# Kernel tuning notes

Measured on AMD Instinct MI355X. Metric: run time of the kernel, lower is better.

## Reference

```python
import jax, jax.numpy as jnp
import numpy as np

B, N1, N2 = 4, 16384, 4096   # scenes, fine points/scene, coarse points/scene
CIN, COUT = 512, 256
K = 3
EPS_BN = 1e-5
EPS_D = 1e-8


def setup_inputs() -> dict:
    key = jax.random.key(0)
    ks = jax.random.split(key, 6)
    return {
        "point_1": jax.random.uniform(ks[0], (B * N1, 3), dtype=jnp.float32),
        "feat_1": jax.random.normal(ks[1], (B * N1, COUT), dtype=jnp.float32) * 0.1,
        "point_2": jax.random.uniform(ks[2], (B * N2, 3), dtype=jnp.float32),
        "feat_2": jax.random.normal(ks[3], (B * N2, CIN), dtype=jnp.float32) * 0.1,
        "W1": jax.random.normal(ks[4], (COUT, COUT), dtype=jnp.float32) / np.sqrt(COUT).astype(np.float32),
        "b1": jnp.zeros((COUT,), jnp.float32),
        "g1": jnp.ones((COUT,), jnp.float32),
        "beta1": jnp.zeros((COUT,), jnp.float32),
        "W2": jax.random.normal(ks[5], (CIN, COUT), dtype=jnp.float32) / np.sqrt(CIN).astype(np.float32),
        "b2": jnp.zeros((COUT,), jnp.float32),
        "g2": jnp.ones((COUT,), jnp.float32),
        "beta2": jnp.zeros((COUT,), jnp.float32),
        # equal-sized segments: row_splits = [0, N, 2N, ...]
        "row_splits_1": jnp.arange(B + 1, dtype=jnp.int32) * N1,
        "row_splits_2": jnp.arange(B + 1, dtype=jnp.int32) * N2,
    }


def _bn(x, gamma, beta):
    # BatchNorm1d, training mode (biased variance, as in torch)
    mu = x.mean(0)
    var = x.var(0)
    return gamma * (x - mu) * jax.lax.rsqrt(var + EPS_BN) + beta


def reference(point_1, feat_1, point_2, feat_2,
              W1, b1, g1, beta1, W2, b2, g2, beta2,
              row_splits_1, row_splits_2):
    # linear1(feat_1): Linear + BN + ReLU
    f1 = jax.nn.relu(_bn(feat_1 @ W1 + b1, g1, beta1))          # [B*N1, COUT]
    # linear2(feat_2): Linear + BN + ReLU
    f2 = jax.nn.relu(_bn(feat_2 @ W2 + b2, g2, beta2))          # [B*N2, COUT]

    # batched KNN (equal row_splits -> reshape into [B, n, 3])
    q = point_1.reshape(B, N1, 3)
    p = point_2.reshape(B, N2, 3)
    d2 = ((q * q).sum(-1)[:, :, None]
          + (p * p).sum(-1)[:, None, :]
          - 2.0 * jnp.einsum("bnd,bmd->bnm", q, p))             # [B, N1, N2] squared dists
    neg_d, idx = jax.lax.top_k(-d2, K)                           # [B, N1, K]
    dist = jnp.maximum(-neg_d, 0.0)

    # inverse-distance weights (knn search is non-differentiable in the original)
    recip = 1.0 / (dist + EPS_D)
    w = jax.lax.stop_gradient(recip / recip.sum(-1, keepdims=True))  # [B, N1, K]

    # gather + weighted sum (three-interpolate)
    f2b = f2.reshape(B, N2, COUT)
    gathered = f2b[jnp.arange(B)[:, None, None], idx]            # [B, N1, K, COUT]
    interp = (gathered * w[..., None]).sum(2).reshape(B * N1, COUT)

    return f1 + interp
```

## Files before the change

kernel.cpp:

```cpp
#include <hip/hip_runtime.h>
#include <hip/hip_bf16.h>
#include <math.h>

#define N1R 65536
#define N2R 16384
#define NPB 4096
#define NQB 16384
#define CC  256
#define KC  64
#define NCELL 512
#define GRID_FAIL_R2 0.015625f

typedef __attribute__((ext_vector_type(4))) float v4f;
typedef __attribute__((ext_vector_type(8))) short v8s;

typedef const __attribute__((address_space(1))) float glb_f32;
typedef __attribute__((address_space(3))) float lds_f32;

static __device__ __forceinline__ void gload16(const float* g, float* l) {
    __builtin_amdgcn_global_load_lds((glb_f32*)g, (lds_f32*)l, 16, 0, 0);
}

static __device__ __forceinline__ short f2bs(float f) {
    union { __hip_bfloat16 h; short s; } u;
    u.h = __float2bfloat16(f);
    return u.s;
}

static __device__ __forceinline__ int cell_of(float x, float y, float z) {
    const int cx = min(7, (int)(x * 8.0f));
    const int cy = min(7, (int)(y * 8.0f));
    const int cz = min(7, (int)(z * 8.0f));
    return (cz << 6) | (cy << 3) | cx;
}

static __device__ __forceinline__ void ins3(float d, int si,
    float& b0, float& b1, float& b2, int& i0, int& i1, int& i2)
{
    const bool lt0 = (d < b0) | ((d == b0) & (si < i0));
    const bool lt1 = (d < b1) | ((d == b1) & (si < i1));
    const bool lt2 = (d < b2) | ((d == b2) & (si < i2));
    b2 = lt1 ? b1 : (lt2 ? d : b2);   i2 = lt1 ? i1 : (lt2 ? si : i2);
    b1 = lt0 ? b0 : (lt1 ? d : b1);   i1 = lt0 ? i0 : (lt1 ? si : i1);
    b0 = lt0 ? d  : b0;               i0 = lt0 ? si : i0;
}

__global__ __launch_bounds__(256)
void wtrans_kernel(const float* __restrict__ W, short* __restrict__ WT, int Kd)
{
    const int i = blockIdx.x * 256 + threadIdx.x;
    const int k = i >> 8;
    const int n = i & 255;
    WT[(size_t)n * Kd + k] = f2bs(W[i]);
}

__global__ __launch_bounds__(256)
void paug_count_kernel(const float* __restrict__ p2, float4* __restrict__ paug,
                       int* __restrict__ counts_p)
{
#pragma clang fp contract(off)
    const int i = blockIdx.x * 256 + threadIdx.x;
    const float x = p2[(size_t)i * 3 + 0];
    const float y = p2[(size_t)i * 3 + 1];
    const float z = p2[(size_t)i * 3 + 2];
    float4 v;
    v.x = x; v.y = y; v.z = z;
    v.w = (x * x + y * y) + z * z;
    paug[i] = v;
    const int b = i >> 12;
    atomicAdd(&counts_p[b * NCELL + cell_of(x, y, z)], 1);
}

__global__ __launch_bounds__(256)
void qcount_kernel(const float* __restrict__ p1, int* __restrict__ counts_q)
{
    const int i = blockIdx.x * 256 + threadIdx.x;
    const float x = p1[(size_t)i * 3 + 0];
    const float y = p1[(size_t)i * 3 + 1];
    const float z = p1[(size_t)i * 3 + 2];
    const int b = i >> 14;
    atomicAdd(&counts_q[b * NCELL + cell_of(x, y, z)], 1);
}

__global__ __launch_bounds__(512)
void prefix_kernel(const int* __restrict__ counts_p, int* __restrict__ cursors_p,
                   int* __restrict__ starts_p,
                   const int* __restrict__ counts_q, int* __restrict__ cursors_q)
{
    __shared__ int sc[512];
    const int t = threadIdx.x;
    for (int a = 0; a < 8; ++a) {
        const int b = a & 3;
        const int* cnt = (a < 4) ? counts_p + b * NCELL : counts_q + b * NCELL;
        const int v = cnt[t];
        sc[t] = v;
        __syncthreads();
        for (int off = 1; off < 512; off <<= 1) {
            const int add = (t >= off) ? sc[t - off] : 0;
            __syncthreads();
            sc[t] += add;
            __syncthreads();
        }
        const int incl = sc[t];
        const int excl = incl - v;
        if (a < 4) {
            starts_p[b * 513 + t] = excl;
            if (t == 511) starts_p[b * 513 + 512] = incl;
            cursors_p[b * NCELL + t] = excl;
        } else {
            cursors_q[b * NCELL + t] = excl;
        }
        __syncthreads();
    }
}

__global__ __launch_bounds__(256)
void scatter_p_kernel(const float4* __restrict__ paug, int* __restrict__ cursors,
                      float4* __restrict__ sortedP, unsigned short* __restrict__ sIdx)
{
    const int i = blockIdx.x * 256 + threadIdx.x;
    const float4 v = paug[i];
    const int b = i >> 12;
    const int cell = cell_of(v.x, v.y, v.z);
    const int pos = atomicAdd(&cursors[b * NCELL + cell], 1);
    sortedP[(size_t)b * NPB + pos] = v;
    sIdx[(size_t)b * NPB + pos] = (unsigned short)(i & 4095);
}

__global__ __launch_bounds__(256)
void scatter_q_kernel(const float* __restrict__ p1, int* __restrict__ cursors,
                      unsigned short* __restrict__ qlist)
{
    const int i = blockIdx.x * 256 + threadIdx.x;
    const float x = p1[(size_t)i * 3 + 0];
    const float y = p1[(size_t)i * 3 + 1];
    const float z = p1[(size_t)i * 3 + 2];
    const int b = i >> 14;
    const int cell = cell_of(x, y, z);
    const int pos = atomicAdd(&cursors[b * NCELL + cell], 1);
    qlist[(size_t)b * NQB + pos] = (unsigned short)(i & 16383);
}

__global__ __launch_bounds__(256)
void gemm_fused_kernel(const float* __restrict__ X,
                       const short* __restrict__ WT,
                       const float* __restrict__ bias,
                       float* __restrict__ Y,
                       float* __restrict__ sum, float* __restrict__ sumsq,
                       int Kdim)
{
    __shared__ float As[2][128 * KC];

    const int bm0 = blockIdx.x * 128;
    const int bn0 = blockIdx.y * 128;
    const int tid  = threadIdx.x;
    const int wave = tid >> 6;
    const int lane = tid & 63;
    const int wm0 = (wave >> 1) * 64;
    const int wn0 = (wave & 1) * 64;
    const int col = lane & 15, quad = lane >> 4;

    const int srow4 = lane >> 4;
    const int sslot = lane & 15;

    v4f acc[4][4];
#pragma unroll
    for (int i = 0; i < 4; ++i)
#pragma unroll
        for (int j = 0; j < 4; ++j) acc[i][j] = (v4f){0.f, 0.f, 0.f, 0.f};

    const short* wbase = WT + (size_t)(bn0 + wn0 + col) * Kdim + quad * 8;

#pragma unroll
    for (int j = 0; j < 8; ++j) {
        const int r = (wave * 8 + j) * 4 + srow4;
        const float* g = X + (size_t)(bm0 + r) * Kdim + ((sslot ^ (r & 7)) << 2);
        gload16(g, &As[0][(wave * 8 + j) * 256]);
    }

    const int NC = Kdim / KC;
    for (int c = 0; c < NC; ++c) {
        const int k0 = c * KC;
        __syncthreads();
        const float* bufc = As[c & 1];

        v8s bf[4][2];
#pragma unroll
        for (int ni = 0; ni < 4; ++ni)
#pragma unroll
            for (int ks = 0; ks < 2; ++ks)
                bf[ni][ks] = *(const v8s*)(wbase + (size_t)(ni * 16) * Kdim + k0 + ks * 32);

        if (c + 1 < NC) {
            float* bufn = As[(c + 1) & 1];
#pragma unroll
            for (int j = 0; j < 8; ++j) {
                const int r = (wave * 8 + j) * 4 + srow4;
                const float* g = X + (size_t)(bm0 + r) * Kdim + (k0 + KC) + ((sslot ^ (r & 7)) << 2);
                gload16(g, &bufn[(wave * 8 + j) * 256]);
            }
        }

#pragma unroll
        for (int ks = 0; ks < 2; ++ks) {
            const int sbase = ks * 8 + quad * 2;
            v8s a[4];
#pragma unroll
            for (int mi = 0; mi < 4; ++mi) {
                const int m = wm0 + mi * 16 + col;
                const float* rowp = bufc + m * KC;
                const v4f pa = *(const v4f*)(rowp + ((sbase ^ (m & 7)) << 2));
                const v4f pb = *(const v4f*)(rowp + (((sbase + 1) ^ (m & 7)) << 2));
                v8s t;
#pragma unroll
                for (int j = 0; j < 4; ++j) { t[j] = f2bs(pa[j]); t[j + 4] = f2bs(pb[j]); }
                a[mi] = t;
            }
#pragma unroll
            for (int mi = 0; mi < 4; ++mi)
#pragma unroll
                for (int ni = 0; ni < 4; ++ni)
                    acc[mi][ni] = __builtin_amdgcn_mfma_f32_16x16x32_bf16(a[mi], bf[ni][ks], acc[mi][ni], 0, 0, 0);
        }
    }

#pragma unroll
    for (int ni = 0; ni < 4; ++ni) {
        const int n = bn0 + wn0 + ni * 16 + col;
        const float bv = bias[n];
        float s = 0.f, q = 0.f;
#pragma unroll
        for (int mi = 0; mi < 4; ++mi) {
            const int m = bm0 + wm0 + mi * 16 + quad * 4;
#pragma unroll
            for (int r = 0; r < 4; ++r) {
                const float y = acc[mi][ni][r] + bv;
                Y[(size_t)(m + r) * CC + n] = y;
                s += y; q += y * y;
            }
        }
        s += __shfl_xor(s, 16); q += __shfl_xor(q, 16);
        s += __shfl_xor(s, 32); q += __shfl_xor(q, 32);
        if (quad == 0) { atomicAdd(&sum[n], s); atomicAdd(&sumsq[n], q); }
    }
}

__global__ __launch_bounds__(512)
void finalize_kernel(const float* __restrict__ sums,
                     const float* __restrict__ g1, const float* __restrict__ be1,
                     const float* __restrict__ g2, const float* __restrict__ be2,
                     float* __restrict__ ac)
{
    const int t = threadIdx.x;
    const int c = t & 255;
    const int which = t >> 8;
    const float* s = sums + which * 512;
    const double n = which ? (double)N2R : (double)N1R;
    const double mu = (double)s[c] / n;
    const double var = (double)s[c + 256] / n - mu * mu;
    const float g  = which ? g2[c]  : g1[c];
    const float be = which ? be2[c] : be1[c];
    const double a  = (double)g / sqrt(var + 1e-5);
    const double cv = (double)be - a * mu;
    ac[which * 512 + c]       = (float)a;
    ac[which * 512 + 256 + c] = (float)cv;
}

__global__ __launch_bounds__(256)
void knn_grid_kernel(const float* __restrict__ p1,
                     const float4* __restrict__ sortedP,
                     const unsigned short* __restrict__ sIdx16,
                     const int* __restrict__ starts_p,
                     const unsigned short* __restrict__ qlist,
                     int* __restrict__ idx_out, float* __restrict__ w_out,
                     int* __restrict__ failCount, int* __restrict__ failList)
{
#pragma clang fp contract(off)
    __shared__ float4 sP[NPB];
    __shared__ unsigned short sI[NPB];
    __shared__ int sS[513];
    __shared__ float mD[128 * 3];
    __shared__ int   mI[128 * 3];

    const int b = blockIdx.x >> 7;
    const int slot0 = (blockIdx.x & 127) * 128;
    const int tid = threadIdx.x;
    const int lq = tid & 127;
    const int half = tid >> 7;

    {
        const float4* gp = sortedP + (size_t)b * NPB;
        for (int i = tid; i < NPB; i += 256) sP[i] = gp[i];
        const unsigned int* gi = (const unsigned int*)(sIdx16 + (size_t)b * NPB);
        unsigned int* li = (unsigned int*)sI;
        for (int i = tid; i < NPB / 2; i += 256) li[i] = gi[i];
        const int* gs = starts_p + b * 513;
        for (int i = tid; i < 513; i += 256) sS[i] = gs[i];
    }

    const int q = qlist[(size_t)b * NQB + slot0 + lq];
    const int qid = b * NQB + q;
    const float qx = p1[(size_t)qid * 3 + 0];
    const float qy = p1[(size_t)qid * 3 + 1];
    const float qz = p1[(size_t)qid * 3 + 2];
    const float qq = (qx * qx + qy * qy) + qz * qz;
    const int cqx = min(7, (int)(qx * 8.0f));
    const int cqy = min(7, (int)(qy * 8.0f));
    const int cqz = min(7, (int)(qz * 8.0f));

    __syncthreads();

    float b0 = 3.0e38f, b1 = 3.0e38f, b2 = 3.0e38f;
    int i0 = 0x7fffffff, i1 = 0x7fffffff, i2 = 0x7fffffff;

    int n = 0;
    for (int dz = -1; dz <= 1; ++dz)
        for (int dy = -1; dy <= 1; ++dy)
            for (int dx = -1; dx <= 1; ++dx, ++n) {
                if (half ? (n < 14) : (n >= 14)) continue;
                const int cz = cqz + dz, cy = cqy + dy, cx = cqx + dx;
                if (((unsigned)cz | (unsigned)cy | (unsigned)cx) > 7u) continue;
                const int cell = (cz << 6) | (cy << 3) | cx;
                const int ks = sS[cell], ke = sS[cell + 1];
                for (int k = ks; k < ke; ++k) {
                    const float4 P = sP[k];
                    const int si = sI[k];
                    const float dot = fmaf(qz, P.z, fmaf(qy, P.y, qx * P.x));
                    const float d = fmaf(-2.0f, dot, qq + P.w);
                    ins3(d, si, b0, b1, b2, i0, i1, i2);
                }
            }

    if (half) {
        mD[lq * 3 + 0] = b0; mD[lq * 3 + 1] = b1; mD[lq * 3 + 2] = b2;
        mI[lq * 3 + 0] = i0; mI[lq * 3 + 1] = i1; mI[lq * 3 + 2] = i2;
    }
    __syncthreads();
    if (!half) {
#pragma unroll
        for (int r = 0; r < 3; ++r)
            ins3(mD[lq * 3 + r], mI[lq * 3 + r], b0, b1, b2, i0, i1, i2);

        if (!(b2 < GRID_FAIL_R2)) {
            const int p = atomicAdd(failCount, 1);
            if (p < N1R) failList[p] = qid;
        }
        const float r0 = 1.0f / (fmaxf(b0, 0.0f) + 1e-8f);
        const float r1 = 1.0f / (fmaxf(b1, 0.0f) + 1e-8f);
        const float r2 = 1.0f / (fmaxf(b2, 0.0f) + 1e-8f);
        const float rs = (r0 + r1) + r2;
        idx_out[(size_t)qid * 3 + 0] = i0;
        idx_out[(size_t)qid * 3 + 1] = i1;
        idx_out[(size_t)qid * 3 + 2] = i2;
        w_out[(size_t)qid * 3 + 0] = r0 / rs;
        w_out[(size_t)qid * 3 + 1] = r1 / rs;
        w_out[(size_t)qid * 3 + 2] = r2 / rs;
    }
}

__global__ __launch_bounds__(256)
void knn_bf_kernel(const float* __restrict__ p1,
                   const float4* __restrict__ paug,
                   const int* __restrict__ failCount,
                   const int* __restrict__ failList,
                   int* __restrict__ idx_out, float* __restrict__ w_out)
{
#pragma clang fp contract(off)
    const int nf = min(*failCount, N1R);
    const int gw = (blockIdx.x * 256 + threadIdx.x) >> 6;
    const int lane = threadIdx.x & 63;
    const int nw = (gridDim.x * 256) >> 6;

    for (int fi = gw; fi < nf; fi += nw) {
        const int qid = failList[fi];
        const int b = qid >> 14;
        const float qx = p1[(size_t)qid * 3 + 0];
        const float qy = p1[(size_t)qid * 3 + 1];
        const float qz = p1[(size_t)qid * 3 + 2];
        const float qq = (qx * qx + qy * qy) + qz * qz;

        float b0 = 3.0e38f, b1 = 3.0e38f, b2 = 3.0e38f;
        int i0 = 0x7fffffff, i1 = 0x7fffffff, i2 = 0x7fffffff;

        const float4* pb = paug + (size_t)b * NPB;
        for (int j = lane; j < NPB; j += 64) {
            const float4 P = pb[j];
            const float dot = fmaf(qz, P.z, fmaf(qy, P.y, qx * P.x));
            const float d = fmaf(-2.0f, dot, qq + P.w);
            ins3(d, j, b0, b1, b2, i0, i1, i2);
        }
        for (int m = 1; m < 64; m <<= 1) {
            const float c0 = __shfl_xor(b0, m), c1 = __shfl_xor(b1, m), c2 = __shfl_xor(b2, m);
            const int j0 = __shfl_xor(i0, m), j1 = __shfl_xor(i1, m), j2 = __shfl_xor(i2, m);
            ins3(c0, j0, b0, b1, b2, i0, i1, i2);
            ins3(c1, j1, b0, b1, b2, i0, i1, i2);
            ins3(c2, j2, b0, b1, b2, i0, i1, i2);
        }
        if (lane == 0) {
            const float r0 = 1.0f / (fmaxf(b0, 0.0f) + 1e-8f);
            const float r1 = 1.0f / (fmaxf(b1, 0.0f) + 1e-8f);
            const float r2 = 1.0f / (fmaxf(b2, 0.0f) + 1e-8f);
            const float rs = (r0 + r1) + r2;
            idx_out[(size_t)qid * 3 + 0] = i0;
            idx_out[(size_t)qid * 3 + 1] = i1;
            idx_out[(size_t)qid * 3 + 2] = i2;
            w_out[(size_t)qid * 3 + 0] = r0 / rs;
            w_out[(size_t)qid * 3 + 1] = r1 / rs;
            w_out[(size_t)qid * 3 + 2] = r2 / rs;
        }
    }
}

__global__ __launch_bounds__(256)
void final_kernel(float* __restrict__ Y1out,
                  const float* __restrict__ Y2raw,
                  const float* __restrict__ ac,
                  const int* __restrict__ idx, const float* __restrict__ w)
{
    const int r = blockIdx.x * 4 + (threadIdx.x >> 6);
    const int cg = threadIdx.x & 63;
    const int b = r >> 14;

    v4f a1 = *(const v4f*)(ac + cg * 4);
    v4f c1 = *(const v4f*)(ac + 256 + cg * 4);
    v4f a2 = *(const v4f*)(ac + 512 + cg * 4);
    v4f c2 = *(const v4f*)(ac + 768 + cg * 4);
    v4f y = *(const v4f*)(Y1out + (size_t)r * CC + cg * 4);
    v4f s;
#pragma unroll
    for (int j = 0; j < 4; ++j)
        s[j] = fmaxf(fmaf(a1[j], y[j], c1[j]), 0.f);

    const int*   ir = idx + (size_t)r * 3;
    const float* wr = w   + (size_t)r * 3;
#pragma unroll
    for (int k = 0; k < 3; ++k) {
        const int id = ir[k];
        const float wk = wr[k];
        v4f g = *(const v4f*)(Y2raw + ((size_t)(b * NPB + id)) * CC + cg * 4);
#pragma unroll
        for (int j = 0; j < 4; ++j) {
            const float gv = fmaxf(fmaf(a2[j], g[j], c2[j]), 0.f);
            s[j] = fmaf(wk, gv, s[j]);
        }
    }
    *(v4f*)(Y1out + (size_t)r * CC + cg * 4) = s;
}

extern "C" void kernel_launch(void* const* d_in, const int* in_sizes, int n_in,
                              void* d_out, int out_size, void* d_ws, size_t ws_size,
                              hipStream_t stream)
{
    const float* point1 = (const float*)d_in[0];
    const float* feat1  = (const float*)d_in[1];
    const float* point2 = (const float*)d_in[2];
    const float* feat2  = (const float*)d_in[3];
    const float* W1     = (const float*)d_in[4];
    const float* b1     = (const float*)d_in[5];
    const float* g1     = (const float*)d_in[6];
    const float* beta1  = (const float*)d_in[7];
    const float* W2     = (const float*)d_in[8];
    const float* b2     = (const float*)d_in[9];
    const float* g2     = (const float*)d_in[10];
    const float* beta2  = (const float*)d_in[11];

    float* Y1 = (float*)d_out;

    char* ws = (char*)d_ws;
    float*          Y2       = (float*)ws;
    float*          stats    = (float*)(ws + (size_t)16777216);
    int*            counts_p = (int*)  (ws + (size_t)16781312);
    int*            counts_q = (int*)  (ws + (size_t)16789504);
    int*            failCnt  = (int*)  (ws + (size_t)16797696);
    int*            cursors_p= (int*)  (ws + (size_t)16801792);
    int*            cursors_q= (int*)  (ws + (size_t)16809984);
    int*            starts_p = (int*)  (ws + (size_t)16818176);
    float*          ac       = (float*)(ws + (size_t)16826624);
    unsigned short* sIdx16   = (unsigned short*)(ws + (size_t)16830720);
    unsigned short* qlist    = (unsigned short*)(ws + (size_t)16863488);
    int*            failList = (int*)  (ws + (size_t)16994560);
    float4*         sortedP  = (float4*)(ws + (size_t)17256704);
    int*            idxb     = (int*)  (ws + (size_t)17518848);
    float*          wb       = (float*)(ws + (size_t)18305280);
    short*          WT1      = (short*)(ws + (size_t)19091712);
    short*          WT2      = (short*)(ws + (size_t)19222784);
    float4*         paug     = (float4*)(ws + (size_t)19484928);

    hipMemsetAsync(stats, 0, 24576, stream);

    wtrans_kernel<<<256, 256, 0, stream>>>(W1, WT1, 256);
    wtrans_kernel<<<512, 256, 0, stream>>>(W2, WT2, 512);

    paug_count_kernel<<<N2R / 256, 256, 0, stream>>>(point2, paug, counts_p);
    qcount_kernel<<<N1R / 256, 256, 0, stream>>>(point1, counts_q);
    prefix_kernel<<<1, 512, 0, stream>>>(counts_p, cursors_p, starts_p, counts_q, cursors_q);
    scatter_p_kernel<<<N2R / 256, 256, 0, stream>>>(paug, cursors_p, sortedP, sIdx16);
    scatter_q_kernel<<<N1R / 256, 256, 0, stream>>>(point1, cursors_q, qlist);

    gemm_fused_kernel<<<dim3(N1R / 128, 2), 256, 0, stream>>>(feat1, WT1, b1, Y1,
                                                              stats + 0,   stats + 256, 256);
    gemm_fused_kernel<<<dim3(N2R / 128, 2), 256, 0, stream>>>(feat2, WT2, b2, Y2,
                                                              stats + 512, stats + 768, 512);

    finalize_kernel<<<1, 512, 0, stream>>>(stats, g1, beta1, g2, beta2, ac);

    knn_grid_kernel<<<512, 256, 0, stream>>>(point1, sortedP, sIdx16, starts_p,
                                             qlist, idxb, wb, failCnt, failList);
    knn_bf_kernel<<<256, 256, 0, stream>>>(point1, paug, failCnt, failList, idxb, wb);

    final_kernel<<<N1R / 4, 256, 0, stream>>>(Y1, Y2, ac, idxb, wb);
}
```

Measured before the change: 350.3 us.

## Load GEMM A operand directly from global into registers, drop LDS staging

The fused GEMM+BN-stats kernel no longer stages the fp32 activation tile in double-buffered LDS via global_load_lds. Each lane now reads its own A fragment straight from global memory, converts it to bf16 and feeds the MFMA. K is also made a template parameter so the loop unrolls at compile time. This removes LDS traffic, barriers and the LDS footprint, which may help occupancy. In exchange, the two column-halves of the grid (blockIdx.y) and the two waves sharing a row range within a block each fetch the same X rows, so global/L2 traffic rises, and latency hiding now depends on unrolling.

Result: slower. 365.3 us (+4.3%).

```diff
diff --git a/kernel.cpp b/kernel.cpp
--- a/kernel.cpp
+++ b/kernel.cpp
@@ -7,19 +7,11 @@
 #define NPB 4096
 #define NQB 16384
 #define CC  256
-#define KC  64
 #define NCELL 512
 #define GRID_FAIL_R2 0.015625f
 
 typedef __attribute__((ext_vector_type(4))) float v4f;
 typedef __attribute__((ext_vector_type(8))) short v8s;
-
-typedef const __attribute__((address_space(1))) float glb_f32;
-typedef __attribute__((address_space(3))) float lds_f32;
-
-static __device__ __forceinline__ void gload16(const float* g, float* l) {
-    __builtin_amdgcn_global_load_lds((glb_f32*)g, (lds_f32*)l, 16, 0, 0);
-}
 
 static __device__ __forceinline__ short f2bs(float f) {
     union { __hip_bfloat16 h; short s; } u;
@@ -141,87 +133,55 @@
     qlist[(size_t)b * NQB + pos] = (unsigned short)(i & 16383);
 }
 
+template<int KD>
 __global__ __launch_bounds__(256)
 void gemm_fused_kernel(const float* __restrict__ X,
                        const short* __restrict__ WT,
                        const float* __restrict__ bias,
                        float* __restrict__ Y,
-                       float* __restrict__ sum, float* __restrict__ sumsq,
-                       int Kdim)
-{
-    __shared__ float As[2][128 * KC];
-
+                       float* __restrict__ sum, float* __restrict__ sumsq)
+{
     const int bm0 = blockIdx.x * 128;
     const int bn0 = blockIdx.y * 128;
-    const int tid  = threadIdx.x;
-    const int wave = tid >> 6;
-    const int lane = tid & 63;
+    const int wave = threadIdx.x >> 6;
+    const int lane = threadIdx.x & 63;
     const int wm0 = (wave >> 1) * 64;
     const int wn0 = (wave & 1) * 64;
     const int col = lane & 15, quad = lane >> 4;
 
-    const int srow4 = lane >> 4;
-    const int sslot = lane & 15;
-
     v4f acc[4][4];
 #pragma unroll
     for (int i = 0; i < 4; ++i)
 #pragma unroll
         for (int j = 0; j < 4; ++j) acc[i][j] = (v4f){0.f, 0.f, 0.f, 0.f};
 
-    const short* wbase = WT + (size_t)(bn0 + wn0 + col) * Kdim + quad * 8;
-
-#pragma unroll
-    for (int j = 0; j < 8; ++j) {
-        const int r = (wave * 8 + j) * 4 + srow4;
-        const float* g = X + (size_t)(bm0 + r) * Kdim + ((sslot ^ (r & 7)) << 2);
-        gload16(g, &As[0][(wave * 8 + j) * 256]);
-    }
-
-    const int NC = Kdim / KC;
-    for (int c = 0; c < NC; ++c) {
-        const int k0 = c * KC;
-        __syncthreads();
-        const float* bufc = As[c & 1];
-
-        v8s bf[4][2];
+    const short* wbase = WT + (size_t)(bn0 + wn0 + col) * KD + quad * 8;
+    const float* xbase = X + (size_t)(bm0 + wm0 + col) * KD + quad * 8;
+
+#pragma unroll 2
+    for (int k0 = 0; k0 < KD; k0 += 32) {
+        v8s bf[4];
 #pragma unroll
         for (int ni = 0; ni < 4; ++ni)
-#pragma unroll
-            for (int ks = 0; ks < 2; ++ks)
-                bf[ni][ks] = *(const v8s*)(wbase + (size_t)(ni * 16) * Kdim + k0 + ks * 32);
-
-        if (c + 1 < NC) {
-            float* bufn = As[(c + 1) & 1];
-#pragma unroll
-            for (int j = 0; j < 8; ++j) {
-                const int r = (wave * 8 + j) * 4 + srow4;
-                const float* g = X + (size_t)(bm0 + r) * Kdim + (k0 + KC) + ((sslot ^ (r & 7)) << 2);
-                gload16(g, &bufn[(wave * 8 + j) * 256]);
-            }
-        }
-
-#pragma unroll
-        for (int ks = 0; ks < 2; ++ks) {
-            const int sbase = ks * 8 + quad * 2;
-            v8s a[4];
-#pragma unroll
-            for (int mi = 0; mi < 4; ++mi) {
-                const int m = wm0 + mi * 16 + col;
-                const float* rowp = bufc + m * KC;
-                const v4f pa = *(const v4f*)(rowp + ((sbase ^ (m & 7)) << 2));
-                const v4f pb = *(const v4f*)(rowp + (((sbase + 1) ^ (m & 7)) << 2));
-                v8s t;
-#pragma unroll
-                for (int j = 0; j < 4; ++j) { t[j] = f2bs(pa[j]); t[j + 4] = f2bs(pb[j]); }
-                a[mi] = t;
-            }
-#pragma unroll
-            for (int mi = 0; mi < 4; ++mi)
-#pragma unroll
-                for (int ni = 0; ni < 4; ++ni)
-                    acc[mi][ni] = __builtin_amdgcn_mfma_f32_16x16x32_bf16(a[mi], bf[ni][ks], acc[mi][ni], 0, 0, 0);
-        }
+            bf[ni] = *(const v8s*)(wbase + (size_t)(ni * 16) * KD + k0);
+
+        v8s a[4];
+#pragma unroll
+        for (int mi = 0; mi < 4; ++mi) {
+            const float* xp = xbase + (size_t)(mi * 16) * KD + k0;
+            const v4f p = *(const v4f*)xp;
+            const v4f q = *(const v4f*)(xp + 4);
+            v8s t;
+#pragma unroll
+            for (int j = 0; j < 4; ++j) { t[j] = f2bs(p[j]); t[j + 4] = f2bs(q[j]); }
+            a[mi] = t;
+        }
+
+#pragma unroll
+        for (int mi = 0; mi < 4; ++mi)
+#pragma unroll
+            for (int ni = 0; ni < 4; ++ni)
+                acc[mi][ni] = __builtin_amdgcn_mfma_f32_16x16x32_bf16(a[mi], bf[ni], acc[mi][ni], 0, 0, 0);
     }
 
 #pragma unroll
@@ -497,10 +457,10 @@
     scatter_p_kernel<<<N2R / 256, 256, 0, stream>>>(paug, cursors_p, sortedP, sIdx16);
     scatter_q_kernel<<<N1R / 256, 256, 0, stream>>>(point1, cursors_q, qlist);
 
-    gemm_fused_kernel<<<dim3(N1R / 128, 2), 256, 0, stream>>>(feat1, WT1, b1, Y1,
-                                                              stats + 0,   stats + 256, 256);
-    gemm_fused_kernel<<<dim3(N2R / 128, 2), 256, 0, stream>>>(feat2, WT2, b2, Y2,
-                                                              stats + 512, stats + 768, 512);
+    gemm_fused_kernel<256><<<dim3(N1R / 128, 2), 256, 0, stream>>>(feat1, WT1, b1, Y1,
+                                                                   stats + 0,   stats + 256);
+    gemm_fused_kernel<512><<<dim3(N2R / 128, 2), 256, 0, stream>>>(feat2, WT2, b2, Y2,
+                                                                   stats + 512, stats + 768);
 
     finalize_kernel<<<1, 512, 0, stream>>>(stats, g1, beta1, g2, beta2, ac);
 
```
